# Kernel tuning notes

Hardware: AMD Instinct MI355X
Metric: run time of the kernel (lower is better)

The kernel has to match this reference:

```python
import jax, jax.numpy as jnp
import numpy as np

D_MODEL = 1024
N_HEADS = 16
HEAD_DIM = D_MODEL // N_HEADS


def setup_inputs() -> dict:
    key = jax.random.key(0)
    kx, kq, kk, kv, ko = jax.random.split(key, 5)
    B, T = 4, 2048
    s = 1.0 / np.sqrt(D_MODEL)
    return {
        "x": jax.random.normal(kx, (B, T, D_MODEL), dtype=jnp.float32),
        "W_Q": jax.random.normal(kq, (D_MODEL, D_MODEL), dtype=jnp.float32) * s,
        "W_K": jax.random.normal(kk, (D_MODEL, D_MODEL), dtype=jnp.float32) * s,
        "W_V": jax.random.normal(kv, (D_MODEL, D_MODEL), dtype=jnp.float32) * s,
        "W_O": jax.random.normal(ko, (D_MODEL, D_MODEL), dtype=jnp.float32) * s,
    }


def reference(x, W_Q, W_K, W_V, W_O):
    B, T, C = x.shape
    H, hd = N_HEADS, HEAD_DIM
    # nn.Linear applies x @ W.T; W_* here are the [out,in] weight matrices.
    def proj(W):
        return (x @ W.T).reshape(B, T, H, hd).transpose(0, 2, 1, 3)  # [B,H,T,hd]
    q, k, v = proj(W_Q), proj(W_K), proj(W_V)
    scale = 1.0 / np.sqrt(hd).astype(np.float32)
    attn = jnp.einsum("bhqd,bhkd->bhqk", q, k) * scale  # [B,H,T,T]
    causal = jnp.tril(jnp.ones((T, T), dtype=bool))
    attn = jnp.where(causal, attn, -jnp.inf)
    attn = jax.nn.softmax(attn, axis=-1)
    out = jnp.einsum("bhqk,bhkd->bhqd", attn, v)  # [B,H,T,hd]
    out = out.transpose(0, 2, 1, 3).reshape(B, T, C)
    return out @ W_O.T
```

## Files before the change

### kernel.cpp

```cpp
#include <hip/hip_runtime.h>
#include <hip/hip_bf16.h>
#include <stdint.h>


typedef __attribute__((ext_vector_type(8))) short short8;
typedef __attribute__((ext_vector_type(4))) short short4v;
typedef __attribute__((ext_vector_type(4))) float floatx4;

#define LOG2E 1.4426950408889634f

__device__ __forceinline__ void gload_lds16(const void* g, void* l) {
  __builtin_amdgcn_global_load_lds(
      (const __attribute__((address_space(1))) void*)g,
      (__attribute__((address_space(3))) void*)l, 16, 0, 0);
}

__device__ __forceinline__ short f2bf(float f) {
  __hip_bfloat16 h = __float2bfloat16(f);
  return *reinterpret_cast<short*>(&h);
}

__global__ __launch_bounds__(256) void cvt_f32_bf16(const float* __restrict__ src,
                                                    short* __restrict__ dst, int n4,
                                                    float scale) {
  const int i = blockIdx.x * blockDim.x + threadIdx.x;
  if (i >= n4) return;
  const float4 v = reinterpret_cast<const float4*>(src)[i];
  short4v o;
  o.x = f2bf(v.x * scale); o.y = f2bf(v.y * scale);
  o.z = f2bf(v.z * scale); o.w = f2bf(v.w * scale);
  reinterpret_cast<short4v*>(dst)[i] = o;
}

__global__ __launch_bounds__(256) void cvt_weights(const float* __restrict__ wq,
                                                   const float* __restrict__ wk,
                                                   const float* __restrict__ wv,
                                                   const float* __restrict__ wo,
                                                   short* __restrict__ dst0,
                                                   float qscale) {
  const int y = blockIdx.y;
  const float* src = (y == 0) ? wq : (y == 1) ? wk : (y == 2) ? wv : wo;
  const float scale = (y == 0) ? qscale : 1.0f;
  short* dst = dst0 + (size_t)y * 1048576;
  const int i = blockIdx.x * blockDim.x + threadIdx.x;
  const float4 v = reinterpret_cast<const float4*>(src)[i];
  short4v o;
  o.x = f2bf(v.x * scale); o.y = f2bf(v.y * scale);
  o.z = f2bf(v.z * scale); o.w = f2bf(v.w * scale);
  reinterpret_cast<short4v*>(&dst[i * 4])[0] = o;
}

template <int MODE>
__device__ __forceinline__ void gemm256_body(const short* __restrict__ A,
                                             const short* __restrict__ B,
                                             void* __restrict__ Cout,
                                             int m0, int n0,
                                             short* __restrict__ la0,
                                             short* __restrict__ la1,
                                             short* __restrict__ la2,
                                             short* __restrict__ lb0,
                                             short* __restrict__ lb1,
                                             short* __restrict__ lb2) {
  const int tid = threadIdx.x;
  const int lane = tid & 63;
  const int w = tid >> 6;
  const int wm = w >> 1, wn = w & 1;
  const int lrow = lane & 15, lgrp = lane >> 4;

  floatx4 acc[4][4] = {};

  const int srow = tid >> 2;
  const int scb = (tid & 3) ^ (srow & 3) ^ ((srow & 4) >> 1);
  const short* ag = A + (size_t)(m0 + srow) * 1024 + scb * 8;
  const short* bg = B + (size_t)(n0 + srow) * 1024 + scb * 8;

  auto stage3 = [&](short* la, short* lb) {
    gload_lds16(ag, la + tid * 8);
    gload_lds16(ag + 128 * 1024, la + (512 + tid) * 8);
    gload_lds16(bg, lb + tid * 8);
    ag += 32; bg += 32;
  };

  const int slA = (lgrp ^ (lrow & 3) ^ ((lrow & 4) >> 1)) * 8;

  auto tile = [&](const short* la, const short* lb, short* na, short* nb, bool pf) {
    if (pf) stage3(na, nb);
    short8 af[4], bf[4];
#pragma unroll
    for (int mf = 0; mf < 4; ++mf) {
      const int row = wm * 64 + mf * 16 + lrow;
      af[mf] = *reinterpret_cast<const short8*>(&la[row * 32 + slA]);
    }
#pragma unroll
    for (int nf = 0; nf < 4; ++nf) {
      const int row = wn * 64 + nf * 16 + lrow;
      bf[nf] = *reinterpret_cast<const short8*>(&lb[row * 32 + slA]);
    }
    __builtin_amdgcn_s_setprio(1);
#pragma unroll
    for (int mf = 0; mf < 4; ++mf)
#pragma unroll
      for (int nf = 0; nf < 4; ++nf)
        acc[mf][nf] = __builtin_amdgcn_mfma_f32_16x16x32_bf16(af[mf], bf[nf], acc[mf][nf], 0, 0, 0);
    __builtin_amdgcn_s_setprio(0);
  };

  auto tiletop = [&](int n) {
    __builtin_amdgcn_sched_barrier(0);
    if (n == 0)
      asm volatile("s_waitcnt vmcnt(0)" ::: "memory");
    else
      asm volatile("s_waitcnt vmcnt(3)" ::: "memory");
    __builtin_amdgcn_s_barrier();
    __builtin_amdgcn_sched_barrier(0);
  };

  stage3(la0, lb0);
  stage3(la1, lb1);

#pragma unroll 1
  for (int kt = 0; kt < 30; kt += 3) {
    tiletop(3); tile(la0, lb0, la2, lb2, true);
    tiletop(3); tile(la1, lb1, la0, lb0, true);
    tiletop(3); tile(la2, lb2, la1, lb1, true);
  }
  tiletop(3); tile(la0, lb0, nullptr, nullptr, false);
  tiletop(0); tile(la1, lb1, nullptr, nullptr, false);

#pragma unroll
  for (int mf = 0; mf < 4; ++mf) {
#pragma unroll
    for (int nf = 0; nf < 4; ++nf) {
      if (MODE == 2) {
        short4v pk;
#pragma unroll
        for (int r = 0; r < 4; ++r) pk[r] = f2bf(acc[mf][nf][r]);
        const int t0 = m0 + wm * 64 + mf * 16 + lgrp * 4;
        const int ch = n0 + wn * 64 + nf * 16 + lrow;
        const int bh = ((t0 >> 11) << 4) + (ch >> 6);
        short* Vt = reinterpret_cast<short*>(Cout);
        *reinterpret_cast<short4v*>(
            &Vt[(size_t)bh * 131072 + (size_t)(ch & 63) * 2048 + (t0 & 2047)]) = pk;
      } else {
#pragma unroll
        for (int r = 0; r < 4; ++r) {
          const int grow = m0 + wm * 64 + mf * 16 + lgrp * 4 + r;
          const int gcol = n0 + wn * 64 + nf * 16 + lrow;
          if (MODE == 1)
            reinterpret_cast<short*>(Cout)[(size_t)grow * 1024 + gcol] = f2bf(acc[mf][nf][r]);
          else
            reinterpret_cast<float*>(Cout)[(size_t)grow * 1024 + gcol] = acc[mf][nf][r];
        }
      }
    }
  }
}

__global__ __launch_bounds__(512) void gemm_qkv(
    const short* __restrict__ xb, const short* __restrict__ wq, const short* __restrict__ wk,
    const short* __restrict__ wv, short* __restrict__ Qb, short* __restrict__ Kb,
    short* __restrict__ Vt) {
  __shared__ short lds_a[3][256 * 32];
  __shared__ short lds_b[3][128 * 32];
  const int flat = blockIdx.x;
  const int xcd = flat & 7, rest = flat >> 3;
  const int nblk = rest & 7, pg = rest >> 3;
  const int panel = pg * 8 + xcd;
  const int m = panel & 31, z = panel >> 5;
  const int m0 = m * 256, n0 = nblk * 128;
  if (z == 0)
    gemm256_body<1>(xb, wq, Qb, m0, n0, lds_a[0], lds_a[1], lds_a[2],
                    lds_b[0], lds_b[1], lds_b[2]);
  else if (z == 1)
    gemm256_body<1>(xb, wk, Kb, m0, n0, lds_a[0], lds_a[1], lds_a[2],
                    lds_b[0], lds_b[1], lds_b[2]);
  else
    gemm256_body<2>(xb, wv, Vt, m0, n0, lds_a[0], lds_a[1], lds_a[2],
                    lds_b[0], lds_b[1], lds_b[2]);
}

__global__ __launch_bounds__(512) void gemm_out(const short* __restrict__ Ob,
                                                const short* __restrict__ wo,
                                                float* __restrict__ out) {
  __shared__ short lds_a[3][256 * 32];
  __shared__ short lds_b[3][128 * 32];
  const int flat = blockIdx.x;
  const int xcd = flat & 7, rest = flat >> 3;
  const int nblk = rest & 7, pg = rest >> 3;
  const int panel = pg * 8 + xcd;
  gemm256_body<0>(Ob, wo, out, panel * 256, nblk * 128,
                  lds_a[0], lds_a[1], lds_a[2], lds_b[0], lds_b[1], lds_b[2]);
}

__global__ __launch_bounds__(256, 4) void attn_fwd(const short* __restrict__ Q,
                                                   const short* __restrict__ K,
                                                   const short* __restrict__ Vt,
                                                   short* __restrict__ O) {
  __shared__ short lds_k[2][64 * 64];
  __shared__ short lds_v[2][64 * 64];
  __shared__ short lds_p[4][16 * 64];

  const int tid = threadIdx.x;
  const int lane = tid & 63;
  const int w = tid >> 6;
  const int lrow = lane & 15, lgrp = lane >> 4;
  const int flat = blockIdx.x;
  const int bh = flat & 63;
  const int p = flat >> 6;
  const int b = bh >> 4, h = bh & 15;

  const size_t base = (size_t)b * 2048 * 1024 + h * 64;
  const size_t vbase = (size_t)bh * 131072;

  const int srow = tid >> 3;
  const int scb = (tid & 7) ^ (srow & 7);
  const size_t koff = (size_t)srow * 1024 + scb * 8;
  const size_t voff = (size_t)srow * 2048 + scb * 8;
  short* const kd0 = &lds_k[0][tid * 8];
  short* const kd1 = &lds_k[1][tid * 8];
  short* const vd0 = &lds_v[0][tid * 8];
  short* const vd1 = &lds_v[1][tid * 8];

  auto stageK = [&](short* ldst, const short* gsrc) {
    gload_lds16(gsrc, ldst);
    gload_lds16(gsrc + 32 * 1024, ldst + 2048);
  };
  auto stageV = [&](short* ldst, const short* gsrc) {
    gload_lds16(gsrc, ldst);
    gload_lds16(gsrc + 32 * 2048, ldst + 2048);
  };

#pragma unroll 1
  for (int pass = 0; pass < 2; ++pass) {
    const int qc = pass == 0 ? (31 - p) : p;
    const int qw = qc * 64 + w * 16;
    const int nkb = qc + 1;

    short8 qf0, qf1;
    {
      const short* qp = Q + base + (size_t)(qw + lrow) * 1024 + lgrp * 8;
      qf0 = *reinterpret_cast<const short8*>(qp);
      qf1 = *reinterpret_cast<const short8*>(qp + 32);
    }

    floatx4 oacc[4] = {};
    float lsum = 0.f;

    const short* kg = K + base + koff;
    const short* vg = Vt + vbase + voff;

    auto body = [&](int kb, const short* __restrict__ ldsk,
                    const short* __restrict__ ldsv) {
      floatx4 s[4];
      __builtin_amdgcn_s_setprio(1);
#pragma unroll
      for (int nf = 0; nf < 4; ++nf) {
        const short8 kf0 = *reinterpret_cast<const short8*>(
            &ldsk[(nf * 16 + lrow) * 64 + ((lgrp) ^ (lrow & 7)) * 8]);
        const short8 kf1 = *reinterpret_cast<const short8*>(
            &ldsk[(nf * 16 + lrow) * 64 + ((4 + lgrp) ^ (lrow & 7)) * 8]);
        floatx4 z = {};
        z = __builtin_amdgcn_mfma_f32_16x16x32_bf16(kf0, qf0, z, 0, 0, 0);
        z = __builtin_amdgcn_mfma_f32_16x16x32_bf16(kf1, qf1, z, 0, 0, 0);
        s[nf] = z;
      }
      __builtin_amdgcn_s_setprio(0);

      if (kb == qc) {
#pragma unroll
        for (int nf = 0; nf < 4; ++nf)
#pragma unroll
          for (int r = 0; r < 4; ++r)
            if (nf * 16 + lgrp * 4 + r > w * 16 + lrow) s[nf][r] = -1e30f;
      }

#pragma unroll
      for (int nf = 0; nf < 4; ++nf) {
        const float p0 = __builtin_amdgcn_exp2f(s[nf][0]);
        const float p1 = __builtin_amdgcn_exp2f(s[nf][1]);
        const float p2 = __builtin_amdgcn_exp2f(s[nf][2]);
        const float p3 = __builtin_amdgcn_exp2f(s[nf][3]);
        lsum += (p0 + p1) + (p2 + p3);
        short4v pk;
        pk.x = f2bf(p0); pk.y = f2bf(p1); pk.z = f2bf(p2); pk.w = f2bf(p3);
        const int c8 = (nf * 4 + lgrp) ^ ((lrow & 7) << 1);
        *reinterpret_cast<short4v*>(&lds_p[w][lrow * 64 + c8 * 4]) = pk;
      }

      short8 pa0, pa1;
      {
        const int c0 = (lgrp) ^ (lrow & 7);
        const int c1 = (4 + lgrp) ^ (lrow & 7);
        pa0 = *reinterpret_cast<const short8*>(&lds_p[w][lrow * 64 + c0 * 8]);
        pa1 = *reinterpret_cast<const short8*>(&lds_p[w][lrow * 64 + c1 * 8]);
      }
      __builtin_amdgcn_s_setprio(1);
#pragma unroll
      for (int nf = 0; nf < 4; ++nf) {
        const short8 vf0 = *reinterpret_cast<const short8*>(
            &ldsv[(nf * 16 + lrow) * 64 + ((lgrp) ^ (lrow & 7)) * 8]);
        const short8 vf1 = *reinterpret_cast<const short8*>(
            &ldsv[(nf * 16 + lrow) * 64 + ((4 + lgrp) ^ (lrow & 7)) * 8]);
        oacc[nf] = __builtin_amdgcn_mfma_f32_16x16x32_bf16(pa0, vf0, oacc[nf], 0, 0, 0);
        oacc[nf] = __builtin_amdgcn_mfma_f32_16x16x32_bf16(pa1, vf1, oacc[nf], 0, 0, 0);
      }
      __builtin_amdgcn_s_setprio(0);
    };

    stageK(kd0, kg); kg += 65536;
    stageV(vd0, vg); vg += 64;
    __syncthreads();

#pragma unroll 1
    for (int kb = 0; kb < nkb; kb += 2) {
      if (kb + 1 < nkb) { stageK(kd1, kg); kg += 65536; stageV(vd1, vg); vg += 64; }
      body(kb, lds_k[0], lds_v[0]);
      __syncthreads();
      if (kb + 1 >= nkb) break;
      if (kb + 2 < nkb) { stageK(kd0, kg); kg += 65536; stageV(vd0, vg); vg += 64; }
      body(kb + 1, lds_k[1], lds_v[1]);
      __syncthreads();
    }

    lsum += __shfl_xor(lsum, 16, 64);
    lsum += __shfl_xor(lsum, 32, 64);
#pragma unroll
    for (int r = 0; r < 4; ++r) {
      const float linv = 1.0f / __shfl(lsum, lgrp * 4 + r, 64);
      const int t = qw + lgrp * 4 + r;
#pragma unroll
      for (int nf = 0; nf < 4; ++nf)
        O[base + (size_t)t * 1024 + nf * 16 + lrow] = f2bf(oacc[nf][r] * linv);
    }
  }
}

extern "C" void kernel_launch(void* const* d_in, const int* in_sizes, int n_in,
                              void* d_out, int out_size, void* d_ws, size_t ws_size,
                              hipStream_t stream) {
  const float* x  = (const float*)d_in[0];
  const float* Wq = (const float*)d_in[1];
  const float* Wk = (const float*)d_in[2];
  const float* Wv = (const float*)d_in[3];
  const float* Wo = (const float*)d_in[4];

  uint8_t* ws = (uint8_t*)d_ws;
  short* xb  = (short*)(ws + 0);
  short* wqb = (short*)(ws + 16777216);
  short* wkb = (short*)(ws + 18874368);
  short* wvb = (short*)(ws + 20971520);
  short* wob = (short*)(ws + 23068672);
  short* Qb  = (short*)(ws + 25165824);
  short* Kb  = (short*)(ws + 41943040);
  short* Vt  = (short*)(ws + 58720256);
  short* Ob  = (short*)(ws + 75497472);
  if (ws_size < 92274688ull) return;

  const float qscale = 0.125f * LOG2E;

  cvt_f32_bf16<<<8192, 256, 0, stream>>>(x, xb, 2097152, 1.0f);
  cvt_weights<<<dim3(1024, 4), 256, 0, stream>>>(Wq, Wk, Wv, Wo, wqb, qscale);

  gemm_qkv<<<768, 512, 0, stream>>>(xb, wqb, wkb, wvb, Qb, Kb, Vt);
  attn_fwd<<<1024, 256, 0, stream>>>(Qb, Kb, Vt, Ob);
  gemm_out<<<256, 512, 0, stream>>>(Ob, wob, (float*)d_out);
}
```

Measured before the change: 158.5 us.

## Enlarge attention query tile to 128 rows with two 16-row subtiles per wave

```diff
diff --git a/kernel.cpp b/kernel.cpp
--- a/kernel.cpp
+++ b/kernel.cpp
@@ -192,13 +192,13 @@
                   lds_a[0], lds_a[1], lds_a[2], lds_b[0], lds_b[1], lds_b[2]);
 }
 
-__global__ __launch_bounds__(256, 4) void attn_fwd(const short* __restrict__ Q,
+__global__ __launch_bounds__(256, 2) void attn_fwd(const short* __restrict__ Q,
                                                    const short* __restrict__ K,
                                                    const short* __restrict__ Vt,
                                                    short* __restrict__ O) {
   __shared__ short lds_k[2][64 * 64];
   __shared__ short lds_v[2][64 * 64];
-  __shared__ short lds_p[4][16 * 64];
+  __shared__ short lds_p[4][2][16 * 64];
 
   const int tid = threadIdx.x;
   const int lane = tid & 63;
@@ -232,26 +232,29 @@
 
 #pragma unroll 1
   for (int pass = 0; pass < 2; ++pass) {
-    const int qc = pass == 0 ? (31 - p) : p;
-    const int qw = qc * 64 + w * 16;
-    const int nkb = qc + 1;
-
-    short8 qf0, qf1;
-    {
-      const short* qp = Q + base + (size_t)(qw + lrow) * 1024 + lgrp * 8;
-      qf0 = *reinterpret_cast<const short8*>(qp);
-      qf1 = *reinterpret_cast<const short8*>(qp + 32);
-    }
-
-    floatx4 oacc[4] = {};
-    float lsum = 0.f;
+    const int qc = pass == 0 ? (15 - p) : p;
+    const int qw = qc * 128 + w * 32;
+    const int lastkb = 2 * qc + (w >> 1);
+    const int nkb = 2 * qc + 2;
+
+    short8 qf[2][2];
+#pragma unroll
+    for (int qt = 0; qt < 2; ++qt) {
+      const short* qp = Q + base + (size_t)(qw + qt * 16 + lrow) * 1024 + lgrp * 8;
+      qf[qt][0] = *reinterpret_cast<const short8*>(qp);
+      qf[qt][1] = *reinterpret_cast<const short8*>(qp + 32);
+    }
+
+    floatx4 oacc[2][4] = {};
+    float lsum0 = 0.f, lsum1 = 0.f;
 
     const short* kg = K + base + koff;
     const short* vg = Vt + vbase + voff;
 
     auto body = [&](int kb, const short* __restrict__ ldsk,
                     const short* __restrict__ ldsv) {
-      floatx4 s[4];
+      if (kb > lastkb) return;
+      floatx4 s[2][4];
       __builtin_amdgcn_s_setprio(1);
 #pragma unroll
       for (int nf = 0; nf < 4; ++nf) {
@@ -259,40 +262,56 @@
             &ldsk[(nf * 16 + lrow) * 64 + ((lgrp) ^ (lrow & 7)) * 8]);
         const short8 kf1 = *reinterpret_cast<const short8*>(
             &ldsk[(nf * 16 + lrow) * 64 + ((4 + lgrp) ^ (lrow & 7)) * 8]);
-        floatx4 z = {};
-        z = __builtin_amdgcn_mfma_f32_16x16x32_bf16(kf0, qf0, z, 0, 0, 0);
-        z = __builtin_amdgcn_mfma_f32_16x16x32_bf16(kf1, qf1, z, 0, 0, 0);
-        s[nf] = z;
+#pragma unroll
+        for (int qt = 0; qt < 2; ++qt) {
+          floatx4 z = {};
+          z = __builtin_amdgcn_mfma_f32_16x16x32_bf16(kf0, qf[qt][0], z, 0, 0, 0);
+          z = __builtin_amdgcn_mfma_f32_16x16x32_bf16(kf1, qf[qt][1], z, 0, 0, 0);
+          s[qt][nf] = z;
+        }
       }
       __builtin_amdgcn_s_setprio(0);
 
-      if (kb == qc) {
-#pragma unroll
-        for (int nf = 0; nf < 4; ++nf)
-#pragma unroll
-          for (int r = 0; r < 4; ++r)
-            if (nf * 16 + lgrp * 4 + r > w * 16 + lrow) s[nf][r] = -1e30f;
-      }
-
-#pragma unroll
-      for (int nf = 0; nf < 4; ++nf) {
-        const float p0 = __builtin_amdgcn_exp2f(s[nf][0]);
-        const float p1 = __builtin_amdgcn_exp2f(s[nf][1]);
-        const float p2 = __builtin_amdgcn_exp2f(s[nf][2]);
-        const float p3 = __builtin_amdgcn_exp2f(s[nf][3]);
-        lsum += (p0 + p1) + (p2 + p3);
-        short4v pk;
-        pk.x = f2bf(p0); pk.y = f2bf(p1); pk.z = f2bf(p2); pk.w = f2bf(p3);
-        const int c8 = (nf * 4 + lgrp) ^ ((lrow & 7) << 1);
-        *reinterpret_cast<short4v*>(&lds_p[w][lrow * 64 + c8 * 4]) = pk;
-      }
-
-      short8 pa0, pa1;
+      if (kb == lastkb) {
+#pragma unroll
+        for (int qt = 0; qt < 2; ++qt)
+#pragma unroll
+          for (int nf = 0; nf < 4; ++nf)
+#pragma unroll
+            for (int r = 0; r < 4; ++r) {
+              const int kg_ = kb * 64 + nf * 16 + lgrp * 4 + r;
+              const int qg_ = qw + qt * 16 + lrow;
+              if (kg_ > qg_) s[qt][nf][r] = -1e30f;
+            }
+      }
+
+#pragma unroll
+      for (int qt = 0; qt < 2; ++qt) {
+        float ls = 0.f;
+#pragma unroll
+        for (int nf = 0; nf < 4; ++nf) {
+          const float p0 = __builtin_amdgcn_exp2f(s[qt][nf][0]);
+          const float p1 = __builtin_amdgcn_exp2f(s[qt][nf][1]);
+          const float p2 = __builtin_amdgcn_exp2f(s[qt][nf][2]);
+          const float p3 = __builtin_amdgcn_exp2f(s[qt][nf][3]);
+          ls += (p0 + p1) + (p2 + p3);
+          short4v pk;
+          pk.x = f2bf(p0); pk.y = f2bf(p1); pk.z = f2bf(p2); pk.w = f2bf(p3);
+          const int c8 = (nf * 4 + lgrp) ^ ((lrow & 7) << 1);
+          *reinterpret_cast<short4v*>(&lds_p[w][qt][lrow * 64 + c8 * 4]) = pk;
+        }
+        if (qt == 0) lsum0 += ls; else lsum1 += ls;
+      }
+
+      short8 pa[2][2];
       {
-        const int c0 = (lgrp) ^ (lrow & 7);
-        const int c1 = (4 + lgrp) ^ (lrow & 7);
-        pa0 = *reinterpret_cast<const short8*>(&lds_p[w][lrow * 64 + c0 * 8]);
-        pa1 = *reinterpret_cast<const short8*>(&lds_p[w][lrow * 64 + c1 * 8]);
+        const int c0 = ((lgrp) ^ (lrow & 7)) * 8;
+        const int c1 = ((4 + lgrp) ^ (lrow & 7)) * 8;
+#pragma unroll
+        for (int qt = 0; qt < 2; ++qt) {
+          pa[qt][0] = *reinterpret_cast<const short8*>(&lds_p[w][qt][lrow * 64 + c0]);
+          pa[qt][1] = *reinterpret_cast<const short8*>(&lds_p[w][qt][lrow * 64 + c1]);
+        }
       }
       __builtin_amdgcn_s_setprio(1);
 #pragma unroll
@@ -301,8 +320,11 @@
             &ldsv[(nf * 16 + lrow) * 64 + ((lgrp) ^ (lrow & 7)) * 8]);
         const short8 vf1 = *reinterpret_cast<const short8*>(
             &ldsv[(nf * 16 + lrow) * 64 + ((4 + lgrp) ^ (lrow & 7)) * 8]);
-        oacc[nf] = __builtin_amdgcn_mfma_f32_16x16x32_bf16(pa0, vf0, oacc[nf], 0, 0, 0);
-        oacc[nf] = __builtin_amdgcn_mfma_f32_16x16x32_bf16(pa1, vf1, oacc[nf], 0, 0, 0);
+#pragma unroll
+        for (int qt = 0; qt < 2; ++qt) {
+          oacc[qt][nf] = __builtin_amdgcn_mfma_f32_16x16x32_bf16(pa[qt][0], vf0, oacc[qt][nf], 0, 0, 0);
+          oacc[qt][nf] = __builtin_amdgcn_mfma_f32_16x16x32_bf16(pa[qt][1], vf1, oacc[qt][nf], 0, 0, 0);
+        }
       }
       __builtin_amdgcn_s_setprio(0);
     };
@@ -322,15 +344,21 @@
       __syncthreads();
     }
 
-    lsum += __shfl_xor(lsum, 16, 64);
-    lsum += __shfl_xor(lsum, 32, 64);
-#pragma unroll
-    for (int r = 0; r < 4; ++r) {
-      const float linv = 1.0f / __shfl(lsum, lgrp * 4 + r, 64);
-      const int t = qw + lgrp * 4 + r;
-#pragma unroll
-      for (int nf = 0; nf < 4; ++nf)
-        O[base + (size_t)t * 1024 + nf * 16 + lrow] = f2bf(oacc[nf][r] * linv);
+    lsum0 += __shfl_xor(lsum0, 16, 64);
+    lsum0 += __shfl_xor(lsum0, 32, 64);
+    lsum1 += __shfl_xor(lsum1, 16, 64);
+    lsum1 += __shfl_xor(lsum1, 32, 64);
+#pragma unroll
+    for (int qt = 0; qt < 2; ++qt) {
+      const float lw = qt == 0 ? lsum0 : lsum1;
+#pragma unroll
+      for (int r = 0; r < 4; ++r) {
+        const float linv = 1.0f / __shfl(lw, lgrp * 4 + r, 64);
+        const int t = qw + qt * 16 + lgrp * 4 + r;
+#pragma unroll
+        for (int nf = 0; nf < 4; ++nf)
+          O[base + (size_t)t * 1024 + nf * 16 + lrow] = f2bf(oacc[qt][nf][r] * linv);
+      }
     }
   }
 }
@@ -362,6 +390,6 @@
   cvt_weights<<<dim3(1024, 4), 256, 0, stream>>>(Wq, Wk, Wv, Wo, wqb, qscale);
 
   gemm_qkv<<<768, 512, 0, stream>>>(xb, wqb, wkb, wvb, Qb, Kb, Vt);
-  attn_fwd<<<1024, 256, 0, stream>>>(Qb, Kb, Vt, Ob);
+  attn_fwd<<<512, 256, 0, stream>>>(Qb, Kb, Vt, Ob);
   gemm_out<<<256, 512, 0, stream>>>(Ob, wob, (float*)d_out);
 }
```

Result: no change. 155.4 us (-1.9%).
